# Kernel tuning notes

Hardware: AMD Instinct MI355X
Metric: run time of the kernel (lower is better)

Reference implementation:

```python
import jax, jax.numpy as jnp
import numpy as np

NPOINT = 2048
RADIUS = 0.2
NSAMPLE = 64
BN_EPS = 1e-5
MLP = [131, 128, 128, 256]  # 128 features + 3 xyz -> 128 -> 128 -> 256


def fps(xyz, npoint):
    """Furthest point sampling. xyz: (B,N,3) -> inds (B,npoint) int32. First index is 0 (CUDA convention)."""
    B, N, _ = xyz.shape
    dist0 = jnp.full((B, N), 1e10, dtype=xyz.dtype)
    idx0 = jnp.zeros((B,), dtype=jnp.int32)

    def step(carry, _):
        dist, last = carry
        last_pt = jnp.take_along_axis(xyz, last[:, None, None].astype(jnp.int32), axis=1)  # (B,1,3)
        d = jnp.sum((xyz - last_pt) ** 2, axis=-1)  # (B,N)
        dist = jnp.minimum(dist, d)
        nxt = jnp.argmax(dist, axis=1).astype(jnp.int32)
        return (dist, nxt), nxt

    (_, _), rest = jax.lax.scan(step, (dist0, idx0), None, length=npoint - 1)
    return jnp.concatenate([idx0[None, :], rest], axis=0).T  # (B,npoint)


def ball_query(all_xyz, new_xyz, radius, nsample):
    """For each query pick the first (lowest-index) nsample points within radius; pad with first hit.
    all_xyz: (B,Np,3), new_xyz: (B,S,3) -> idx (B,S,nsample) int32."""
    Np = all_xyz.shape[1]
    d2 = jnp.sum((new_xyz[:, :, None, :] - all_xyz[:, None, :, :]) ** 2, axis=-1)  # (B,S,Np)
    key = jnp.where(d2 < radius * radius, jnp.arange(Np, dtype=jnp.int32)[None, None, :], Np)
    topk = -jax.lax.top_k(-key, nsample)[0]  # nsample smallest indices, ascending
    valid = topk < Np
    first = topk[..., :1]
    idx = jnp.where(valid, topk, first)
    return jnp.where(idx >= Np, 0, idx).astype(jnp.int32)


def bn_relu(x, gamma, beta):
    # training-mode BatchNorm over (B,S,K) per channel (last axis), biased variance
    mean = jnp.mean(x, axis=(0, 1, 2), keepdims=True)
    var = jnp.mean((x - mean) ** 2, axis=(0, 1, 2), keepdims=True)
    return jax.nn.relu((x - mean) * jax.lax.rsqrt(var + BN_EPS) * gamma + beta)


def setup_inputs() -> dict:
    key = jax.random.key(0)
    ks = jax.random.split(key, 10)
    B, N, M, C = 4, 16384, 256, 128
    fixed_xyz = jax.random.uniform(ks[0], (B, M, 3), dtype=jnp.float32)
    xyz = jax.random.uniform(ks[1], (B, N, 3), dtype=jnp.float32)
    features = jax.random.normal(ks[2], (B, C, M + N), dtype=jnp.float32)
    W1 = jax.random.normal(ks[3], (MLP[1], MLP[0]), dtype=jnp.float32) * 0.05
    W2 = jax.random.normal(ks[4], (MLP[2], MLP[1]), dtype=jnp.float32) * 0.05
    W3 = jax.random.normal(ks[5], (MLP[3], MLP[2]), dtype=jnp.float32) * 0.05
    g1 = jnp.ones((MLP[1],), jnp.float32); b1 = jnp.zeros((MLP[1],), jnp.float32)
    g2 = jnp.ones((MLP[2],), jnp.float32); b2 = jnp.zeros((MLP[2],), jnp.float32)
    g3 = jnp.ones((MLP[3],), jnp.float32); b3 = jnp.zeros((MLP[3],), jnp.float32)
    return {"fixed_xyz": fixed_xyz, "xyz": xyz, "features": features,
            "W1": W1, "g1": g1, "b1": b1, "W2": W2, "g2": g2, "b2": b2,
            "W3": W3, "g3": g3, "b3": b3}


def reference(fixed_xyz, xyz, features, W1, g1, b1, W2, g2, b2, W3, g3, b3):
    B = xyz.shape[0]
    # FPS on the raw cloud, gather sampled centers, prepend fixed seeds
    inds = fps(xyz, NPOINT)  # (B,npoint)
    sampled = jnp.take_along_axis(xyz, inds[:, :, None], axis=1)  # (B,npoint,3)
    new_xyz = jnp.concatenate([fixed_xyz, sampled], axis=1)       # (B,S,3)
    all_xyz = jnp.concatenate([fixed_xyz, xyz], axis=1)           # (B,Np,3)

    idx = ball_query(all_xyz, new_xyz, RADIUS, NSAMPLE)           # (B,S,K)
    b = jnp.arange(B)[:, None, None]
    grouped_xyz = all_xyz[b, idx] - new_xyz[:, :, None, :]        # (B,S,K,3)
    grouped_xyz = grouped_xyz / RADIUS                            # normalize_xyz=True
    feats_t = jnp.transpose(features, (0, 2, 1))                  # (B,Np,C)
    grouped_feats = feats_t[b, idx]                               # (B,S,K,C)
    h = jnp.concatenate([grouped_xyz, grouped_feats], axis=-1)    # (B,S,K,3+C)

    # Shared MLP: 1x1 conv (no bias) + BN + ReLU per layer
    h = bn_relu(jnp.einsum('bskc,oc->bsko', h, W1), g1, b1)
    h = bn_relu(jnp.einsum('bskc,oc->bsko', h, W2), g2, b2)
    h = bn_relu(jnp.einsum('bskc,oc->bsko', h, W3), g3, b3)

    # max pool over the K (nsample) axis -> (B,Cout,S)
    new_features = jnp.transpose(jnp.max(h, axis=2), (0, 2, 1))
    return new_xyz, new_features, inds
```

## Files before the change

kernel.cpp:

```cpp
#include <hip/hip_runtime.h>
#include <hip/hip_bf16.h>
#include <cstdint>
#include <cstddef>

#define NB 4
#define N_PTS 16384
#define M_FIX 256
#define P_ALL 16640
#define S_TOT 2304
#define NPT 2048
#define KNB 64
#define CH1 128
#define CH3 256
#define NRED 589824.0f

typedef float v2f __attribute__((ext_vector_type(2)));

#define OUT_XYZ 0
#define OUT_FEAT 27648
#define OUT_INDS 2386944

#define OFF_ALLX   0ull
#define OFF_STATS  798720ull
#define OFF_BN     1060864ull
#define OFF_MAXZ   1064960ull
#define OFF_MINZ   10502144ull
#define OFF_IDX    19939328ull
#define OFF_ZP     22298624ull
#define OFF_NEWX   39337984ull
#define OFF_INDSI  39448576ull
#define OFF_HIST   1064960ull
#define OFF_OFFS   1073152ull
#define OFF_SX     1081344ull
#define OFF_SY     1343488ull
#define OFF_SZ     1605632ull
#define OFF_SIDX   1867776ull
#define OFF_XYZ4   2129920ull

__device__ __forceinline__ float red16s(float v) {
  v += __shfl_xor(v, 1); v += __shfl_xor(v, 2);
  v += __shfl_xor(v, 4); v += __shfl_xor(v, 8);
  return v;
}
__device__ __forceinline__ float red16mx(float v) {
  v = fmaxf(v, __shfl_xor(v, 1)); v = fmaxf(v, __shfl_xor(v, 2));
  v = fmaxf(v, __shfl_xor(v, 4)); v = fmaxf(v, __shfl_xor(v, 8));
  return v;
}
__device__ __forceinline__ float red16mn(float v) {
  v = fminf(v, __shfl_xor(v, 1)); v = fminf(v, __shfl_xor(v, 2));
  v = fminf(v, __shfl_xor(v, 4)); v = fminf(v, __shfl_xor(v, 8));
  return v;
}
__device__ __forceinline__ float xyzp(float dx, float dy, float dz,
                                      float wx, float wy, float wz) {
  return fmaf(dx, wx, fmaf(dy, wy, __fmul_rn(dz, wz)));
}
__device__ __forceinline__ int mort3(int v) {
  return (v & 1) | ((v & 2) << 1) | ((v & 4) << 2);
}
__device__ __forceinline__ int cell_code(float x, float y, float z) {
  int cx = min(7, max(0, (int)(x * 8.0f)));
  int cy = min(7, max(0, (int)(y * 8.0f)));
  int cz = min(7, max(0, (int)(z * 8.0f)));
  return mort3(cx) | (mort3(cy) << 1) | (mort3(cz) << 2);
}

template <int CTRL, int RM>
__device__ __forceinline__ unsigned long long dppmax(unsigned long long k) {
  int lo = (int)(unsigned)(k & 0xFFFFFFFFull);
  int hi = (int)(unsigned)(k >> 32);
  int sl = __builtin_amdgcn_update_dpp(lo, lo, CTRL, RM, 0xF, false);
  int sh = __builtin_amdgcn_update_dpp(hi, hi, CTRL, RM, 0xF, false);
  unsigned long long s = ((unsigned long long)(unsigned)sh << 32) | (unsigned)sl;
  return (s > k) ? s : k;
}
__device__ __forceinline__ unsigned long long wave_max64(unsigned long long k) {
  k = dppmax<0x111, 0xF>(k);
  k = dppmax<0x112, 0xF>(k);
  k = dppmax<0x114, 0xF>(k);
  k = dppmax<0x118, 0xF>(k);
  k = dppmax<0x142, 0xa>(k);
  k = dppmax<0x143, 0xc>(k);
  return k;
}
__device__ __forceinline__ unsigned long long row_max64(unsigned long long k) {
  k = dppmax<0x111, 0xF>(k);
  k = dppmax<0x112, 0xF>(k);
  k = dppmax<0x114, 0xF>(k);
  k = dppmax<0x118, 0xF>(k);
  return k;
}

__global__ void k_build(const float* __restrict__ fixed, const float* __restrict__ xyz,
                        float* __restrict__ allx, float* __restrict__ newx,
                        float* __restrict__ stats, int* __restrict__ inds_i,
                        int* __restrict__ hist, float4* __restrict__ xyz4) {
  int i = blockIdx.x * 256 + threadIdx.x;
  if (i < NB * P_ALL * 3) {
    int b = i / (P_ALL * 3);
    int r = i % (P_ALL * 3);
    int p = r / 3, c = r % 3;
    float v = (p < M_FIX) ? fixed[((size_t)b * M_FIX + p) * 3 + c]
                          : xyz[((size_t)b * N_PTS + (p - M_FIX)) * 3 + c];
    allx[i] = v;
  }
  if (i < NB * N_PTS) {
    const float* pt = xyz + (size_t)i * 3;
    xyz4[i] = make_float4(pt[0], pt[1], pt[2], 0.f);
  }
  if (i < NB * M_FIX * 3) {
    int b = i / (M_FIX * 3);
    int r = i % (M_FIX * 3);
    newx[(size_t)b * S_TOT * 3 + r] = fixed[(size_t)b * M_FIX * 3 + r];
  }
  if (i < 65536) stats[i] = 0.0f;
  if (i < NB * 512) hist[i] = 0;
  if (i < NB) inds_i[(size_t)i * NPT] = 0;
}

__global__ void k_cell(const float* __restrict__ xyz, int* __restrict__ hist) {
  int i = blockIdx.x * 256 + threadIdx.x;
  int b = i >> 14;
  const float* pt = xyz + (size_t)i * 3;
  int code = cell_code(pt[0], pt[1], pt[2]);
  atomicAdd(&hist[(b << 9) + code], 1);
}

__global__ __launch_bounds__(512) void k_scan(const int* __restrict__ hist,
                                              int* __restrict__ offs) {
  __shared__ int tmp[512];
  int b = blockIdx.x, t = threadIdx.x;
  int h = hist[(b << 9) + t];
  tmp[t] = h;
  __syncthreads();
  for (int o = 1; o < 512; o <<= 1) {
    int v = (t >= o) ? tmp[t - o] : 0;
    __syncthreads();
    tmp[t] += v;
    __syncthreads();
  }
  offs[(b << 9) + t] = tmp[t] - h;
}

__global__ void k_scatter(const float* __restrict__ xyz, int* __restrict__ offs,
                          float* __restrict__ sx, float* __restrict__ sy,
                          float* __restrict__ sz, int* __restrict__ sidx) {
  int i = blockIdx.x * 256 + threadIdx.x;
  int b = i >> 14, p = i & 16383;
  const float* pt = xyz + (size_t)i * 3;
  float x = pt[0], y = pt[1], z = pt[2];
  int code = cell_code(x, y, z);
  int pos = atomicAdd(&offs[(b << 9) + code], 1);
  int o = (b << 14) + pos;
  sx[o] = x; sy[o] = y; sz[o] = z; sidx[o] = p;
}

__global__ __launch_bounds__(1024, 4) void k_fps(const float4* __restrict__ xyz4,
                                                 const float* __restrict__ sx,
                                                 const float* __restrict__ sy,
                                                 const float* __restrict__ sz,
                                                 const int* __restrict__ sidx,
                                                 float* __restrict__ newx,
                                                 int* __restrict__ inds_i) {
  int b = blockIdx.x, t = threadIdx.x;
  const float4* bx4 = xyz4 + (size_t)b * N_PTS;
  int off0 = (b << 14) + (t << 4);
  v2f px2[8], py2[8], pz2[8];
  float dist[16];
  unsigned npidp[8];
#pragma unroll
  for (int u = 0; u < 8; ++u) {
    px2[u] = *(const v2f*)&sx[off0 + 2 * u];
    py2[u] = *(const v2f*)&sy[off0 + 2 * u];
    pz2[u] = *(const v2f*)&sz[off0 + 2 * u];
    dist[2 * u] = 1e10f; dist[2 * u + 1] = 1e10f;
  }
#pragma unroll
  for (int u = 0; u < 8; ++u) {
    unsigned a = 16383u - (unsigned)sidx[off0 + 2 * u];
    unsigned c = 16383u - (unsigned)sidx[off0 + 2 * u + 1];
    npidp[u] = a | (c << 16);
  }
  float xmn = px2[0].x, xmx = px2[0].x, ymn = py2[0].x, ymx = py2[0].x;
  float zmn = pz2[0].x, zmx = pz2[0].x;
#pragma unroll
  for (int u = 0; u < 8; ++u) {
    xmn = fminf(xmn, fminf(px2[u].x, px2[u].y));
    xmx = fmaxf(xmx, fmaxf(px2[u].x, px2[u].y));
    ymn = fminf(ymn, fminf(py2[u].x, py2[u].y));
    ymx = fmaxf(ymx, fmaxf(py2[u].x, py2[u].y));
    zmn = fminf(zmn, fminf(pz2[u].x, pz2[u].y));
    zmx = fmaxf(zmx, fmaxf(pz2[u].x, pz2[u].y));
  }
  float cx = (xmn + xmx) * 0.5f, cy = (ymn + ymx) * 0.5f, cz = (zmn + zmx) * 0.5f;
  float r2m = 0.f;
#pragma unroll
  for (int u = 0; u < 8; ++u) {
#pragma unroll
    for (int h = 0; h < 2; ++h) {
      float ax = (h ? px2[u].y : px2[u].x) - cx;
      float ay = (h ? py2[u].y : py2[u].x) - cy;
      float az = (h ? pz2[u].y : pz2[u].x) - cz;
      r2m = fmaxf(r2m, ax * ax + ay * ay + az * az);
    }
  }
  float rad = sqrtf(r2m) + 2e-3f;
  float4 p0 = bx4[0];
  float lx = p0.x, ly = p0.y, lz = p0.z;
  if (t == 0) {
    size_t nb0 = ((size_t)b * S_TOT + M_FIX) * 3;
    newx[nb0] = lx; newx[nb0 + 1] = ly; newx[nb0 + 2] = lz;
  }
  __shared__ unsigned long long red[16];
  __shared__ __align__(16) float4 wcoord[16];
  __shared__ __align__(16) float4 s_win;
  __shared__ int idxbuf[NPT];
  unsigned long long bestkey = 0ull;
  unsigned long long kprev = ~0ull;
  float thr = 3.4e38f;
  int lane = t & 63, wid = t >> 6;
  for (int iter = 1; iter < NPT; ++iter) {
    float ex = lx - cx, ey = ly - cy, ez = lz - cz;
    bool active = (ex * ex + ey * ey + ez * ez) < thr;
    if (__ballot(active) != 0ull) {
      bool ch = false;
      if (active) {
#pragma clang fp contract(off)
        v2f l2x = {lx, lx}, l2y = {ly, ly}, l2z = {lz, lz};
#pragma unroll
        for (int u = 0; u < 8; ++u) {
          v2f dx = px2[u] - l2x;
          v2f dy = py2[u] - l2y;
          v2f dz = pz2[u] - l2z;
          v2f xx = dx * dx;
          v2f yy = dy * dy;
          v2f zz = dz * dz;
          v2f d2 = (xx + yy) + zz;
          if (d2.x < dist[2 * u])     { dist[2 * u] = d2.x;     ch = true; }
          if (d2.y < dist[2 * u + 1]) { dist[2 * u + 1] = d2.y; ch = true; }
        }
      }
      if (__ballot(ch) != 0ull) {
        if (ch) {
          unsigned long long c0 = 0ull, c1 = 0ull, c2 = 0ull, c3 = 0ull;
#pragma unroll
          for (int j = 0; j < 16; ++j) {
            unsigned lo16 = (j & 1) ? (npidp[j >> 1] >> 16) : (npidp[j >> 1] & 0xFFFFu);
            unsigned long long kj =
                ((unsigned long long)__float_as_uint(dist[j]) << 32) | lo16;
            if ((j & 3) == 0) c0 = (kj > c0) ? kj : c0;
            else if ((j & 3) == 1) c1 = (kj > c1) ? kj : c1;
            else if ((j & 3) == 2) c2 = (kj > c2) ? kj : c2;
            else c3 = (kj > c3) ? kj : c3;
          }
          c0 = (c1 > c0) ? c1 : c0;
          c2 = (c3 > c2) ? c3 : c2;
          bestkey = (c2 > c0) ? c2 : c0;
          float ub = __uint_as_float((unsigned)(bestkey >> 32));
          float tq = sqrtf(ub) + rad;
          thr = tq * tq;
        }
        unsigned long long k = wave_max64(bestkey);
        unsigned long long kall = __shfl(k, 63);
        if (kall != kprev) {
          if (bestkey == kall) {
            unsigned lo = (unsigned)(kall & 0xFFFFull);
            float wx = 0.f, wy = 0.f, wz = 0.f;
#pragma unroll
            for (int u = 0; u < 8; ++u) {
              unsigned pk = npidp[u];
              if ((pk & 0xFFFFu) == lo) { wx = px2[u].x; wy = py2[u].x; wz = pz2[u].x; }
              if ((pk >> 16) == lo)     { wx = px2[u].y; wy = py2[u].y; wz = pz2[u].y; }
            }
            wcoord[wid] = make_float4(wx, wy, wz, 0.f);
          }
          kprev = kall;
        }
        if (lane == 63) red[wid] = k;
      }
    }
    __syncthreads();
    if (wid == 0) {
      unsigned long long wk = red[lane & 15];
      unsigned long long wr = row_max64(wk);
      unsigned long long wmax = __shfl(wr, 15);
      unsigned long long mb = __ballot(wk == wmax) & 0xFFFFull;
      int src = __ffsll(mb) - 1;
      if (lane == 15) {
        s_win = wcoord[src];
        idxbuf[iter] = 16383 - (int)(wmax & 0xFFFFull);
      }
    }
    __syncthreads();
    float4 wv = s_win;
    lx = wv.x; ly = wv.y; lz = wv.z;
  }
  __syncthreads();
  for (int s = t; s < NPT; s += 1024) {
    if (s == 0) continue;
    int wi = idxbuf[s];
    float4 wp = bx4[wi];
    inds_i[(size_t)b * NPT + s] = wi;
    size_t nb2 = ((size_t)b * S_TOT + M_FIX + s) * 3;
    newx[nb2] = wp.x; newx[nb2 + 1] = wp.y; newx[nb2 + 2] = wp.z;
  }
}

__global__ __launch_bounds__(256) void k_ball(const float* __restrict__ allx,
                                              const float* __restrict__ newx,
                                              int* __restrict__ idx) {
  int wid = threadIdx.x >> 6, lane = threadIdx.x & 63;
  int q = blockIdx.x * 4 + wid;
  int b = q / S_TOT;
  const float* qp = newx + (size_t)q * 3;
  float qx = qp[0], qy = qp[1], qz = qp[2];
  const float* pts = allx + (size_t)b * P_ALL * 3;
  int* outp = idx + (size_t)q * KNB;
  const float R2 = 0.04f;
  int collected = 0;
  int first_hit = 0;
  for (int ch = 0; ch < P_ALL / 64; ++ch) {
    int p = ch * 64 + lane;
    float x = pts[p * 3 + 0], y = pts[p * 3 + 1], z = pts[p * 3 + 2];
    float dx = __fsub_rn(qx, x), dy = __fsub_rn(qy, y), dz = __fsub_rn(qz, z);
    float d2 = __fadd_rn(__fadd_rn(__fmul_rn(dx, dx), __fmul_rn(dy, dy)), __fmul_rn(dz, dz));
    bool hit = d2 < R2;
    unsigned long long m = __ballot(hit);
    if (m) {
      if (collected == 0) first_hit = ch * 64 + (__ffsll((unsigned long long)m) - 1);
      if (hit) {
        int slot = collected + __popcll(m & ((1ull << lane) - 1ull));
        if (slot < KNB) outp[slot] = p;
      }
      collected += __popcll(m);
      if (collected >= KNB) break;
    }
  }
  int sl = collected + lane;
  if (sl < KNB) outp[sl] = first_hit;
}

__device__ __forceinline__ void gemm_chunks(const float* a_t, float* w_t,
                                            const float* __restrict__ Wg, int K,
                                            int obase, int ldw, int tid,
                                            v2f acc[4][4]) {
  int tk = tid & 15, to = tid >> 4;
  for (int c0 = 0; c0 < K; c0 += 32) {
    __syncthreads();
    for (int r = tid; r < 32 * 128; r += 256) {
      int o = r & 127, c = r >> 7;
      w_t[c * 132 + o] = Wg[(size_t)(obase + o) * ldw + (c0 + c)];
    }
    __syncthreads();
#pragma unroll 4
    for (int c = 0; c < 32; ++c) {
      float a4[4];
      v2f w2[4];
      *(float4*)a4 = *(const float4*)&a_t[(c0 + c) * 68 + tk * 4];
      *(float4*)&w2[0] = *(const float4*)&w_t[c * 132 + to * 8];
      *(float4*)&w2[2] = *(const float4*)&w_t[c * 132 + to * 8 + 4];
#pragma unroll
      for (int i = 0; i < 4; ++i) {
        v2f a2 = {a4[i], a4[i]};
#pragma unroll
        for (int p = 0; p < 4; ++p)
          acc[i][p] = __builtin_elementwise_fma(a2, w2[p], acc[i][p]);
      }
    }
  }
}
#define ACC_J(acc, i, j) (((j) & 1) ? acc[i][(j) >> 1].y : acc[i][(j) >> 1].x)

__global__ __launch_bounds__(256) void k_zp(const float* __restrict__ feats,
                                            const float* __restrict__ W1,
                                            __hip_bfloat16* __restrict__ zp) {
  __shared__ __align__(16) float smem[CH1 * 68 + 32 * 132];
  float* a_t = smem;
  float* w_t = smem + CH1 * 68;
  int b = blockIdx.y;
  int p0 = blockIdx.x * 64;
  int tid = threadIdx.x;
  for (int r = tid; r < CH1 * 64; r += 256) {
    int c = r >> 6, p = r & 63;
    a_t[c * 68 + p] = feats[((size_t)b * CH1 + c) * P_ALL + p0 + p];
  }
  v2f acc[4][4];
#pragma unroll
  for (int i = 0; i < 4; ++i)
#pragma unroll
    for (int p = 0; p < 4; ++p) acc[i][p] = (v2f){0.f, 0.f};
  gemm_chunks(a_t, w_t, W1 + 3, CH1, 0, 131, tid, acc);
  int tk = tid & 15, to = tid >> 4;
#pragma unroll
  for (int i = 0; i < 4; ++i) {
    int p = p0 + tk * 4 + i;
    union { __hip_bfloat16 h[8]; uint4 u; } tmp;
#pragma unroll
    for (int j = 0; j < 8; ++j) tmp.h[j] = __float2bfloat16(ACC_J(acc, i, j));
    *(uint4*)&zp[((size_t)b * P_ALL + p) * CH1 + to * 8] = tmp.u;
  }
}

__device__ __forceinline__ void stage_geom(int bs, int b, const int* __restrict__ idxg,
                                           const float* __restrict__ allx,
                                           const float* __restrict__ newx,
                                           const float* __restrict__ W1,
                                           int* s_pid, float* s_d, float* s_w1, int tid) {
  if (tid < 64) {
    int p = idxg[(size_t)bs * KNB + tid];
    s_pid[tid] = p;
    const float* pp = allx + ((size_t)b * P_ALL + p) * 3;
    const float* qq = newx + (size_t)bs * 3;
    s_d[tid]       = __fmul_rn(__fsub_rn(pp[0], qq[0]), 5.0f);
    s_d[64 + tid]  = __fmul_rn(__fsub_rn(pp[1], qq[1]), 5.0f);
    s_d[128 + tid] = __fmul_rn(__fsub_rn(pp[2], qq[2]), 5.0f);
  } else if (tid < 192) {
    int c = tid - 64;
    s_w1[c]       = W1[(size_t)c * 131 + 0];
    s_w1[128 + c] = W1[(size_t)c * 131 + 1];
    s_w1[256 + c] = W1[(size_t)c * 131 + 2];
  }
  __syncthreads();
}

__global__ __launch_bounds__(256) void k_stats1(const int* __restrict__ idxg,
                                                const float* __restrict__ allx,
                                                const float* __restrict__ newx,
                                                const float* __restrict__ W1,
                                                const __hip_bfloat16* __restrict__ zp,
                                                float* __restrict__ sSum,
                                                float* __restrict__ sSq) {
  __shared__ float smem[640 + 512];
  int* s_pid = (int*)smem;
  float* s_d = smem + 64;
  float* s_w1 = smem + 256;
  float* red = smem + 640;
  int bs = blockIdx.x;
  int b = bs / S_TOT;
  int tid = threadIdx.x;
  stage_geom(bs, b, idxg, allx, newx, W1, s_pid, s_d, s_w1, tid);
  int g = tid >> 7, c = tid & 127;
  float wx = s_w1[c], wy = s_w1[128 + c], wz = s_w1[256 + c];
  const uint16_t* zpb = (const uint16_t*)zp + (size_t)b * P_ALL * CH1;
  float s1 = 0.f, s2 = 0.f;
  for (int k = g; k < KNB; k += 2) {
    int pid = s_pid[k];
    float v = __uint_as_float(((unsigned)zpb[(size_t)pid * CH1 + c]) << 16);
    v += xyzp(s_d[k], s_d[64 + k], s_d[128 + k], wx, wy, wz);
    s1 += v; s2 = fmaf(v, v, s2);
  }
  red[tid] = s1;
  __syncthreads();
  float t1 = (tid < 128) ? red[tid] + red[tid + 128] : 0.f;
  __syncthreads();
  red[tid] = s2;
  __syncthreads();
  if (tid < 128) {
    float t2 = red[tid] + red[tid + 128];
    int slot = bs & 63;
    atomicAdd(&sSum[slot * CH1 + tid], t1);
    atomicAdd(&sSq[slot * CH1 + tid], t2);
  }
}

__device__ __forceinline__ void build_a1(float* a_t, const int* s_pid, const float* s_d,
                                         const float* s_w1,
                                         const __hip_bfloat16* __restrict__ zp_b,
                                         const float* __restrict__ bnS,
                                         const float* __restrict__ bnH, int tid) {
  int k = tid & 63, q = tid >> 6;
  int pid = s_pid[k];
  float dx = s_d[k], dy = s_d[64 + k], dz = s_d[128 + k];
  const uint32_t* zr = (const uint32_t*)((const uint16_t*)zp_b + (size_t)pid * CH1 + q * 32);
#pragma unroll
  for (int u = 0; u < 16; ++u) {
    uint32_t w = zr[u];
    int c = q * 32 + u * 2;
    float v0 = __uint_as_float(w << 16);
    float v1 = __uint_as_float(w & 0xFFFF0000u);
    v0 += xyzp(dx, dy, dz, s_w1[c], s_w1[128 + c], s_w1[256 + c]);
    v1 += xyzp(dx, dy, dz, s_w1[c + 1], s_w1[128 + c + 1], s_w1[256 + c + 1]);
    a_t[c * 68 + k]       = fmaxf(fmaf(v0, bnS[c], bnH[c]), 0.0f);
    a_t[(c + 1) * 68 + k] = fmaxf(fmaf(v1, bnS[c + 1], bnH[c + 1]), 0.0f);
  }
}

__global__ __launch_bounds__(256) void k_layer2s(const int* __restrict__ idxg,
                                                 const float* __restrict__ allx,
                                                 const float* __restrict__ newx,
                                                 const float* __restrict__ W1,
                                                 const __hip_bfloat16* __restrict__ zp,
                                                 const float* __restrict__ bn1S,
                                                 const float* __restrict__ bn1H,
                                                 const float* __restrict__ W2,
                                                 float* __restrict__ sSum,
                                                 float* __restrict__ sSq) {
  __shared__ __align__(16) float smem[CH1 * 68 + 32 * 132];
  float* a_t = smem;
  float* w_t = smem + CH1 * 68;
  int* s_pid = (int*)w_t;
  float* s_d = w_t + 64;
  float* s_w1 = w_t + 256;
  int bs = blockIdx.x;
  int b = bs / S_TOT;
  int tid = threadIdx.x;
  stage_geom(bs, b, idxg, allx, newx, W1, s_pid, s_d, s_w1, tid);
  build_a1(a_t, s_pid, s_d, s_w1, zp + (size_t)b * P_ALL * CH1, bn1S, bn1H, tid);
  v2f acc[4][4];
#pragma unroll
  for (int i = 0; i < 4; ++i)
#pragma unroll
    for (int p = 0; p < 4; ++p) acc[i][p] = (v2f){0.f, 0.f};
  gemm_chunks(a_t, w_t, W2, CH1, 0, CH1, tid, acc);
  int tk = tid & 15, to = tid >> 4;
  int slot = bs & 63;
#pragma unroll
  for (int j = 0; j < 8; ++j) {
    float s1 = 0.f, s2 = 0.f;
#pragma unroll
    for (int i = 0; i < 4; ++i) { float v = ACC_J(acc, i, j); s1 += v; s2 = fmaf(v, v, s2); }
    s1 = red16s(s1);
    s2 = red16s(s2);
    if (tk == 0) {
      int o = to * 8 + j;
      atomicAdd(&sSum[slot * CH1 + o], s1);
      atomicAdd(&sSq[slot * CH1 + o], s2);
    }
  }
}

__global__ __launch_bounds__(256) void k_layer3(const int* __restrict__ idxg,
                                                const float* __restrict__ allx,
                                                const float* __restrict__ newx,
                                                const float* __restrict__ W1,
                                                const __hip_bfloat16* __restrict__ zp,
                                                const float* __restrict__ bn1S,
                                                const float* __restrict__ bn1H,
                                                const float* __restrict__ W2,
                                                const float* __restrict__ bn2S,
                                                const float* __restrict__ bn2H,
                                                const float* __restrict__ W3,
                                                float* __restrict__ maxz,
                                                float* __restrict__ minz,
                                                float* __restrict__ sSum,
                                                float* __restrict__ sSq) {
  __shared__ __align__(16) float smem[CH1 * 68 + 32 * 132];
  float* a_t = smem;
  float* w_t = smem + CH1 * 68;
  int* s_pid = (int*)w_t;
  float* s_d = w_t + 64;
  float* s_w1 = w_t + 256;
  int bs = blockIdx.x;
  int b = bs / S_TOT;
  int tid = threadIdx.x;
  stage_geom(bs, b, idxg, allx, newx, W1, s_pid, s_d, s_w1, tid);
  build_a1(a_t, s_pid, s_d, s_w1, zp + (size_t)b * P_ALL * CH1, bn1S, bn1H, tid);
  v2f acc[4][4];
#pragma unroll
  for (int i = 0; i < 4; ++i)
#pragma unroll
    for (int p = 0; p < 4; ++p) acc[i][p] = (v2f){0.f, 0.f};
  gemm_chunks(a_t, w_t, W2, CH1, 0, CH1, tid, acc);
  int tk = tid & 15, to = tid >> 4;
  __syncthreads();
#pragma unroll
  for (int j = 0; j < 8; ++j) {
    int o = to * 8 + j;
    float sc = bn2S[o], sh = bn2H[o];
#pragma unroll
    for (int i = 0; i < 4; ++i)
      a_t[o * 68 + tk * 4 + i] = fmaxf(fmaf(ACC_J(acc, i, j), sc, sh), 0.0f);
  }
  int slot = bs & 63;
#pragma unroll 1
  for (int half = 0; half < 2; ++half) {
    v2f acc3[4][4];
#pragma unroll
    for (int i = 0; i < 4; ++i)
#pragma unroll
      for (int p = 0; p < 4; ++p) acc3[i][p] = (v2f){0.f, 0.f};
    gemm_chunks(a_t, w_t, W3, CH1, half * 128, CH1, tid, acc3);
#pragma unroll
    for (int j = 0; j < 8; ++j) {
      float s1 = 0.f, s2 = 0.f, mx = -3.4e38f, mn = 3.4e38f;
#pragma unroll
      for (int i = 0; i < 4; ++i) {
        float v = ACC_J(acc3, i, j);
        s1 += v; s2 = fmaf(v, v, s2);
        mx = fmaxf(mx, v); mn = fminf(mn, v);
      }
      s1 = red16s(s1);
      s2 = red16s(s2);
      mx = red16mx(mx);
      mn = red16mn(mn);
      if (tk == 0) {
        int o = half * 128 + to * 8 + j;
        atomicAdd(&sSum[slot * CH3 + o], s1);
        atomicAdd(&sSq[slot * CH3 + o], s2);
        size_t base = (size_t)bs * CH3 + o;
        maxz[base] = mx;
        minz[base] = mn;
      }
    }
  }
}

__global__ void k_fin(const float* __restrict__ sSum, const float* __restrict__ sSq,
                      const float* __restrict__ gamma, const float* __restrict__ beta,
                      float* __restrict__ bnS, float* __restrict__ bnH, int C) {
  int o = threadIdx.x;
  if (o >= C) return;
  float s1 = 0.f, s2 = 0.f;
  for (int t = 0; t < 64; ++t) { s1 += sSum[t * C + o]; s2 += sSq[t * C + o]; }
  float mean = s1 / NRED;
  float var = fmaxf(s2 / NRED - mean * mean, 0.f);
  float inv = 1.0f / sqrtf(var + 1e-5f);
  float sc = gamma[o] * inv;
  bnS[o] = sc;
  bnH[o] = beta[o] - mean * sc;
}

__global__ __launch_bounds__(256) void k_final(const float* __restrict__ maxz,
                                               const float* __restrict__ minz,
                                               const float* __restrict__ bnS,
                                               const float* __restrict__ bnH,
                                               float* __restrict__ out) {
  int bs = blockIdx.x;
  int o = threadIdx.x;
  float sc = bnS[o], sh = bnH[o];
  size_t base = (size_t)bs * CH3 + o;
  float v = (sc >= 0.f) ? maxz[base] : minz[base];
  float r = fmaxf(fmaf(v, sc, sh), 0.f);
  int b = bs / S_TOT, s = bs % S_TOT;
  out[OUT_FEAT + ((size_t)b * CH3 + o) * S_TOT + s] = r;
}

__global__ void k_copy(const float* __restrict__ newx, const int* __restrict__ inds_i,
                       float* __restrict__ out) {
  int i = blockIdx.x * 256 + threadIdx.x;
  if (i < NB * S_TOT * 3) out[OUT_XYZ + i] = newx[i];
  else {
    int r = i - NB * S_TOT * 3;
    if (r < NB * NPT) out[OUT_INDS + r] = (float)inds_i[r];
  }
}

extern "C" void kernel_launch(void* const* d_in, const int* in_sizes, int n_in,
                              void* d_out, int out_size, void* d_ws, size_t ws_size,
                              hipStream_t stream) {
  const float* fixed = (const float*)d_in[0];
  const float* xyz = (const float*)d_in[1];
  const float* feats = (const float*)d_in[2];
  const float* W1 = (const float*)d_in[3];
  const float* g1 = (const float*)d_in[4];
  const float* b1 = (const float*)d_in[5];
  const float* W2 = (const float*)d_in[6];
  const float* g2 = (const float*)d_in[7];
  const float* b2 = (const float*)d_in[8];
  const float* W3 = (const float*)d_in[9];
  const float* g3 = (const float*)d_in[10];
  const float* b3 = (const float*)d_in[11];
  float* out = (float*)d_out;

  char* w = (char*)d_ws;
  float* allx = (float*)(w + OFF_ALLX);
  float* newx = (float*)(w + OFF_NEWX);
  int* inds_i = (int*)(w + OFF_INDSI);
  int* idx = (int*)(w + OFF_IDX);
  float* stats = (float*)(w + OFF_STATS);
  float* s1sum = stats, *s1sq = stats + 8192;
  float* s2sum = stats + 16384, *s2sq = stats + 24576;
  float* s3sum = stats + 32768, *s3sq = stats + 49152;
  float* bn = (float*)(w + OFF_BN);
  float* bn1s = bn, *bn1h = bn + 128;
  float* bn2s = bn + 256, *bn2h = bn + 384;
  float* bn3s = bn + 512, *bn3h = bn + 768;
  float* maxz = (float*)(w + OFF_MAXZ);
  float* minz = (float*)(w + OFF_MINZ);
  __hip_bfloat16* zp = (__hip_bfloat16*)(w + OFF_ZP);
  int* hist = (int*)(w + OFF_HIST);
  int* offs = (int*)(w + OFF_OFFS);
  float* sxp = (float*)(w + OFF_SX);
  float* syp = (float*)(w + OFF_SY);
  float* szp = (float*)(w + OFF_SZ);
  int* sidx = (int*)(w + OFF_SIDX);
  float4* xyz4 = (float4*)(w + OFF_XYZ4);

  k_build<<<(NB * P_ALL * 3 + 255) / 256, 256, 0, stream>>>(fixed, xyz, allx, newx, stats, inds_i, hist, xyz4);
  k_cell<<<NB * N_PTS / 256, 256, 0, stream>>>(xyz, hist);
  k_scan<<<NB, 512, 0, stream>>>(hist, offs);
  k_scatter<<<NB * N_PTS / 256, 256, 0, stream>>>(xyz, offs, sxp, syp, szp, sidx);
  k_fps<<<NB, 1024, 0, stream>>>(xyz4, sxp, syp, szp, sidx, newx, inds_i);
  k_ball<<<(NB * S_TOT) / 4, 256, 0, stream>>>(allx, newx, idx);
  k_zp<<<dim3(P_ALL / 64, NB), 256, 0, stream>>>(feats, W1, zp);
  k_stats1<<<NB * S_TOT, 256, 0, stream>>>(idx, allx, newx, W1, zp, s1sum, s1sq);
  k_fin<<<1, 256, 0, stream>>>(s1sum, s1sq, g1, b1, bn1s, bn1h, 128);
  k_layer2s<<<NB * S_TOT, 256, 0, stream>>>(idx, allx, newx, W1, zp, bn1s, bn1h, W2, s2sum, s2sq);
  k_fin<<<1, 256, 0, stream>>>(s2sum, s2sq, g2, b2, bn2s, bn2h, 128);
  k_layer3<<<NB * S_TOT, 256, 0, stream>>>(idx, allx, newx, W1, zp, bn1s, bn1h, W2,
                                           bn2s, bn2h, W3, maxz, minz, s3sum, s3sq);
  k_fin<<<1, 256, 0, stream>>>(s3sum, s3sq, g3, b3, bn3s, bn3h, 256);
  k_final<<<NB * S_TOT, 256, 0, stream>>>(maxz, minz, bn3s, bn3h, out);
  k_copy<<<(NB * S_TOT * 3 + NB * NPT + 255) / 256, 256, 0, stream>>>(newx, inds_i, out);
}
```

Before: 4.645 ms.

## Fuse feature projection GEMM into FPS launch to overlap with serial FPS

```diff
diff --git a/kernel.cpp b/kernel.cpp
--- a/kernel.cpp
+++ b/kernel.cpp
@@ -13,6 +13,7 @@
 #define CH1 128
 #define CH3 256
 #define NRED 589824.0f
+#define ZPB (P_ALL / 64)
 
 typedef float v2f __attribute__((ext_vector_type(2)));
 
@@ -162,8 +163,61 @@
                                                  const float* __restrict__ sz,
                                                  const int* __restrict__ sidx,
                                                  float* __restrict__ newx,
-                                                 int* __restrict__ inds_i) {
-  int b = blockIdx.x, t = threadIdx.x;
+                                                 int* __restrict__ inds_i,
+                                                 const float* __restrict__ feats,
+                                                 const float* __restrict__ W1,
+                                                 __hip_bfloat16* __restrict__ zp) {
+  __shared__ __align__(16) float smem[CH1 * 68 + 32 * 132];
+  int t = threadIdx.x;
+
+  if (blockIdx.x >= NB) {
+    int bz = blockIdx.x - NB;
+    int b = bz / ZPB;
+    int p0 = (bz % ZPB) * 64;
+    float* a_t = smem;
+    float* w_t = smem + CH1 * 68;
+    for (int r = t; r < CH1 * 64; r += 1024) {
+      int c = r >> 6, p = r & 63;
+      a_t[c * 68 + p] = feats[((size_t)b * CH1 + c) * P_ALL + p0 + p];
+    }
+    int tk = t & 63, to = t >> 6;
+    v2f acc[4];
+#pragma unroll
+    for (int p = 0; p < 4; ++p) acc[p] = (v2f){0.f, 0.f};
+    const float* Wg = W1 + 3;
+    for (int c0 = 0; c0 < CH1; c0 += 32) {
+      __syncthreads();
+      for (int r = t; r < 32 * 128; r += 1024) {
+        int o = r & 127, c = r >> 7;
+        w_t[c * 132 + o] = Wg[(size_t)o * 131 + (c0 + c)];
+      }
+      __syncthreads();
+#pragma unroll 4
+      for (int c = 0; c < 32; ++c) {
+        float a = a_t[(c0 + c) * 68 + tk];
+        v2f w2[4];
+        *(float4*)&w2[0] = *(const float4*)&w_t[c * 132 + to * 8];
+        *(float4*)&w2[2] = *(const float4*)&w_t[c * 132 + to * 8 + 4];
+        v2f a2 = {a, a};
+#pragma unroll
+        for (int p = 0; p < 4; ++p)
+          acc[p] = __builtin_elementwise_fma(a2, w2[p], acc[p]);
+      }
+    }
+    union { __hip_bfloat16 h[8]; uint4 u; } tmp;
+#pragma unroll
+    for (int j = 0; j < 8; ++j)
+      tmp.h[j] = __float2bfloat16((j & 1) ? acc[j >> 1].y : acc[j >> 1].x);
+    *(uint4*)&zp[((size_t)b * P_ALL + p0 + tk) * CH1 + to * 8] = tmp.u;
+    return;
+  }
+
+  unsigned long long* red = (unsigned long long*)smem;
+  float4* wcoord = (float4*)(smem + 32);
+  float4* s_win = (float4*)(smem + 96);
+  int* idxbuf = (int*)(smem + 100);
+
+  int b = blockIdx.x;
   const float4* bx4 = xyz4 + (size_t)b * N_PTS;
   int off0 = (b << 14) + (t << 4);
   v2f px2[8], py2[8], pz2[8];
@@ -212,10 +266,6 @@
     size_t nb0 = ((size_t)b * S_TOT + M_FIX) * 3;
     newx[nb0] = lx; newx[nb0 + 1] = ly; newx[nb0 + 2] = lz;
   }
-  __shared__ unsigned long long red[16];
-  __shared__ __align__(16) float4 wcoord[16];
-  __shared__ __align__(16) float4 s_win;
-  __shared__ int idxbuf[NPT];
   unsigned long long bestkey = 0ull;
   unsigned long long kprev = ~0ull;
   float thr = 3.4e38f;
@@ -288,12 +338,12 @@
       unsigned long long mb = __ballot(wk == wmax) & 0xFFFFull;
       int src = __ffsll(mb) - 1;
       if (lane == 15) {
-        s_win = wcoord[src];
+        *s_win = wcoord[src];
         idxbuf[iter] = 16383 - (int)(wmax & 0xFFFFull);
       }
     }
     __syncthreads();
-    float4 wv = s_win;
+    float4 wv = *s_win;
     lx = wv.x; ly = wv.y; lz = wv.z;
   }
   __syncthreads();
@@ -371,36 +421,6 @@
   }
 }
 #define ACC_J(acc, i, j) (((j) & 1) ? acc[i][(j) >> 1].y : acc[i][(j) >> 1].x)
-
-__global__ __launch_bounds__(256) void k_zp(const float* __restrict__ feats,
-                                            const float* __restrict__ W1,
-                                            __hip_bfloat16* __restrict__ zp) {
-  __shared__ __align__(16) float smem[CH1 * 68 + 32 * 132];
-  float* a_t = smem;
-  float* w_t = smem + CH1 * 68;
-  int b = blockIdx.y;
-  int p0 = blockIdx.x * 64;
-  int tid = threadIdx.x;
-  for (int r = tid; r < CH1 * 64; r += 256) {
-    int c = r >> 6, p = r & 63;
-    a_t[c * 68 + p] = feats[((size_t)b * CH1 + c) * P_ALL + p0 + p];
-  }
-  v2f acc[4][4];
-#pragma unroll
-  for (int i = 0; i < 4; ++i)
-#pragma unroll
-    for (int p = 0; p < 4; ++p) acc[i][p] = (v2f){0.f, 0.f};
-  gemm_chunks(a_t, w_t, W1 + 3, CH1, 0, 131, tid, acc);
-  int tk = tid & 15, to = tid >> 4;
-#pragma unroll
-  for (int i = 0; i < 4; ++i) {
-    int p = p0 + tk * 4 + i;
-    union { __hip_bfloat16 h[8]; uint4 u; } tmp;
-#pragma unroll
-    for (int j = 0; j < 8; ++j) tmp.h[j] = __float2bfloat16(ACC_J(acc, i, j));
-    *(uint4*)&zp[((size_t)b * P_ALL + p) * CH1 + to * 8] = tmp.u;
-  }
-}
 
 __device__ __forceinline__ void stage_geom(int bs, int b, const int* __restrict__ idxg,
                                            const float* __restrict__ allx,
@@ -691,9 +711,9 @@
   k_cell<<<NB * N_PTS / 256, 256, 0, stream>>>(xyz, hist);
   k_scan<<<NB, 512, 0, stream>>>(hist, offs);
   k_scatter<<<NB * N_PTS / 256, 256, 0, stream>>>(xyz, offs, sxp, syp, szp, sidx);
-  k_fps<<<NB, 1024, 0, stream>>>(xyz4, sxp, syp, szp, sidx, newx, inds_i);
+  k_fps<<<NB + NB * ZPB, 1024, 0, stream>>>(xyz4, sxp, syp, szp, sidx, newx, inds_i,
+                                            feats, W1, zp);
   k_ball<<<(NB * S_TOT) / 4, 256, 0, stream>>>(allx, newx, idx);
-  k_zp<<<dim3(P_ALL / 64, NB), 256, 0, stream>>>(feats, W1, zp);
   k_stats1<<<NB * S_TOT, 256, 0, stream>>>(idx, allx, newx, W1, zp, s1sum, s1sq);
   k_fin<<<1, 256, 0, stream>>>(s1sum, s1sq, g1, b1, bn1s, bn1h, 128);
   k_layer2s<<<NB * S_TOT, 256, 0, stream>>>(idx, allx, newx, W1, zp, bn1s, bn1h, W2, s2sum, s2sq);
```

After: 4.587 ms. Within noise of the previous version (-1.3%).
